# Performance work log

Measured on AMD Instinct MI355X. Metric: run time of the kernel, lower is better.

## Reference

```python
import jax, jax.numpy as jnp
import numpy as np

B, S, IN_F, OUT_F = 4, 2048, 4096, 4096
LUT_SIZE = 256


def setup_inputs() -> dict:
    key = jax.random.key(0)
    k_x, k_idx = jax.random.split(key, 2)
    x = jax.random.normal(k_x, (B, S, IN_F), dtype=jnp.float32)
    # quantized weight codes, one per weight element (uint8 in torch; int32 here)
    grid_indices = jax.random.randint(k_idx, (OUT_F, IN_F), 0, LUT_SIZE, dtype=jnp.int32)
    # per-output-row scale, initialized to ones as in the module
    scale = jnp.ones((OUT_F, 1), dtype=jnp.float32)
    # PRIMAL_LUT: 256-entry linear manifold codebook
    lut = jnp.linspace(-1.0, 1.0, LUT_SIZE, dtype=jnp.float32)
    return {"x": x, "grid_indices": grid_indices, "scale": scale, "lut": lut}


def reference(x, grid_indices, scale, lut):
    # dequant: gather codebook entries per weight element, scale per output row
    weights = lut[grid_indices] * scale            # [OUT_F, IN_F]
    # F.linear(x, weights) == x @ weights.T
    return jnp.einsum('bsi,oi->bso', x, weights)   # [B, S, OUT_F]
```

## Files before the change

kernel.cpp:

```cpp
#include <hip/hip_runtime.h>
#include <hip/hip_bf16.h>


#define M_DIM 8192
#define N_DIM 4096
#define K_DIM 4096
#define BM 128
#define BN 128
#define BK 64

typedef __bf16 bf16x8 __attribute__((ext_vector_type(8)));
typedef float floatx4 __attribute__((ext_vector_type(4)));
typedef int intx4 __attribute__((ext_vector_type(4)));
typedef unsigned short ushortx8 __attribute__((ext_vector_type(8)));

__device__ __forceinline__ unsigned short f2bf(float f) {
    return __builtin_bit_cast(unsigned short, (__bf16)f);
}

__device__ __forceinline__ void async_load16(const void* g, void* l) {
    auto gp = reinterpret_cast<const __attribute__((address_space(1))) void*>(
        reinterpret_cast<unsigned long long>(g));
    auto lp = reinterpret_cast<__attribute__((address_space(3))) void*>(
        static_cast<unsigned int>(reinterpret_cast<unsigned long long>(l)));
    __builtin_amdgcn_global_load_lds(gp, lp, 16, 0, 0);
}

__global__ __launch_bounds__(256) void prep(const float* __restrict__ x,
                                            unsigned short* __restrict__ xb,
                                            const int* __restrict__ idx,
                                            const float* __restrict__ scale,
                                            const float* __restrict__ lut,
                                            unsigned short* __restrict__ wb) {
    __shared__ float slut[256];
    if (blockIdx.x < 16384) {
        size_t i = ((size_t)blockIdx.x * 256 + threadIdx.x) * 8;
        floatx4 a = __builtin_nontemporal_load((const floatx4*)(x + i));
        floatx4 b = __builtin_nontemporal_load((const floatx4*)(x + i + 4));
        ushortx8 v;
        v[0] = f2bf(a[0]); v[1] = f2bf(a[1]); v[2] = f2bf(a[2]); v[3] = f2bf(a[3]);
        v[4] = f2bf(b[0]); v[5] = f2bf(b[1]); v[6] = f2bf(b[2]); v[7] = f2bf(b[3]);
        *(ushortx8*)(xb + i) = v;
    } else {
        if (threadIdx.x < 256) slut[threadIdx.x] = lut[threadIdx.x];
        __syncthreads();
        size_t i = ((size_t)(blockIdx.x - 16384) * 256 + threadIdx.x) * 8;
        int row = (int)(i >> 12);
        float s = scale[row];
        intx4 i0 = __builtin_nontemporal_load((const intx4*)(idx + i));
        intx4 i1 = __builtin_nontemporal_load((const intx4*)(idx + i + 4));
        ushortx8 v;
        v[0] = f2bf(slut[i0[0]] * s); v[1] = f2bf(slut[i0[1]] * s);
        v[2] = f2bf(slut[i0[2]] * s); v[3] = f2bf(slut[i0[3]] * s);
        v[4] = f2bf(slut[i1[0]] * s); v[5] = f2bf(slut[i1[1]] * s);
        v[6] = f2bf(slut[i1[2]] * s); v[7] = f2bf(slut[i1[3]] * s);
        *(ushortx8*)(wb + i) = v;
    }
}

__global__ __launch_bounds__(256) void gemm_bf16(const unsigned short* __restrict__ A,
                                                 const unsigned short* __restrict__ Bw,
                                                 float* __restrict__ C) {
    __shared__ __align__(16) unsigned short As[BM * BK];
    __shared__ __align__(16) unsigned short Bs[BN * BK];

    const int id = blockIdx.x;
    const int st = id >> 5;
    const int li = id & 31;
    const int m_blk = (st & 7) * 8 + (li & 7);
    const int n_blk = (st >> 3) * 4 + (li >> 3);
    const int m0 = m_blk * BM;
    const int n0 = n_blk * BN;

    const int t    = threadIdx.x;
    const int wave = t >> 6;
    const int lane = t & 63;

    const int mw   = (wave >> 1) * 64;
    const int nw   = (wave & 1) * 64;
    const int quad = lane >> 4;
    const int lcol = lane & 15;

    floatx4 acc[4][4];
#pragma unroll
    for (int i = 0; i < 4; i++)
#pragma unroll
        for (int j = 0; j < 4; j++) acc[i][j] = (floatx4)0.0f;

    const int rr = t >> 3;
    const int cc = t & 7;
    const int sw = (((cc - rr) & 7) << 3);
    unsigned short* AsB[4];
    unsigned short* BsB[4];
#pragma unroll
    for (int i = 0; i < 4; i++) {
        AsB[i] = As + (i * 32 + (wave << 3)) * BK;
        BsB[i] = Bs + (i * 32 + (wave << 3)) * BK;
    }

    const unsigned short* aG = A + (size_t)m0 * K_DIM;
    const unsigned short* bG = Bw + (size_t)n0 * K_DIM;

    for (int k0 = 0; k0 < K_DIM; k0 += BK) {
#pragma unroll
        for (int i = 0; i < 4; i++) {
            async_load16(aG + (size_t)(i * 32 + rr) * K_DIM + k0 + sw, AsB[i]);
            async_load16(bG + (size_t)(i * 32 + rr) * K_DIM + k0 + sw, BsB[i]);
        }
        __syncthreads();

#pragma unroll
        for (int ks = 0; ks < 2; ks++) {
            bf16x8 a[4], b[4];
#pragma unroll
            for (int mt = 0; mt < 4; mt++) {
                int R = mw + mt * 16 + lcol;
                int ch = (quad + ks * 4 + R) & 7;
                a[mt] = *(const bf16x8*)(As + R * BK + ch * 8);
            }
#pragma unroll
            for (int nt = 0; nt < 4; nt++) {
                int R = nw + nt * 16 + lcol;
                int ch = (quad + ks * 4 + R) & 7;
                b[nt] = *(const bf16x8*)(Bs + R * BK + ch * 8);
            }
#pragma unroll
            for (int mt = 0; mt < 4; mt++)
#pragma unroll
                for (int nt = 0; nt < 4; nt++)
                    acc[mt][nt] = __builtin_amdgcn_mfma_f32_16x16x32_bf16(
                        a[mt], b[nt], acc[mt][nt], 0, 0, 0);
        }
        __syncthreads();
    }

#pragma unroll
    for (int mt = 0; mt < 4; mt++) {
#pragma unroll
        for (int r = 0; r < 4; r++) {
            int row = m0 + mw + mt * 16 + quad * 4 + r;
            float* cr = C + (size_t)row * N_DIM + n0 + nw + lcol;
#pragma unroll
            for (int nt = 0; nt < 4; nt++)
                __builtin_nontemporal_store(acc[mt][nt][r], cr + nt * 16);
        }
    }
}

__global__ __launch_bounds__(256) void gemm_fallback(const float* __restrict__ x,
                                                     const int* __restrict__ idx,
                                                     const float* __restrict__ scale,
                                                     const float* __restrict__ lut,
                                                     float* __restrict__ C) {
    __shared__ float xs[16][17];
    __shared__ float wsm[16][17];
    const int tx = threadIdx.x & 15;
    const int ty = threadIdx.x >> 4;
    const int m = blockIdx.y * 16 + ty;
    const int n = blockIdx.x * 16 + tx;
    float acc = 0.f;
    for (int k0 = 0; k0 < K_DIM; k0 += 16) {
        xs[ty][tx] = x[(size_t)m * K_DIM + k0 + tx];
        int wrow = blockIdx.x * 16 + ty;
        wsm[ty][tx] = lut[idx[(size_t)wrow * K_DIM + k0 + tx]] * scale[wrow];
        __syncthreads();
#pragma unroll
        for (int kk = 0; kk < 16; kk++) acc += xs[ty][kk] * wsm[tx][kk];
        __syncthreads();
    }
    C[(size_t)m * N_DIM + n] = acc;
}

extern "C" void kernel_launch(void* const* d_in, const int* in_sizes, int n_in,
                              void* d_out, int out_size, void* d_ws, size_t ws_size,
                              hipStream_t stream) {
    const float* x     = (const float*)d_in[0];
    const int*   gidx  = (const int*)d_in[1];
    const float* scale = (const float*)d_in[2];
    const float* lut   = (const float*)d_in[3];
    float*       out   = (float*)d_out;

    const size_t needA = (size_t)M_DIM * K_DIM * sizeof(unsigned short);
    const size_t needW = (size_t)N_DIM * K_DIM * sizeof(unsigned short);

    if (ws_size >= needA + needW) {
        unsigned short* Ab = (unsigned short*)d_ws;
        unsigned short* Wb = Ab + (size_t)M_DIM * K_DIM;
        prep<<<24576, 256, 0, stream>>>(x, Ab, gidx, scale, lut, Wb);
        gemm_bf16<<<(M_DIM / BM) * (N_DIM / BN), 256, 0, stream>>>(Ab, Wb, out);
    } else {
        dim3 grid(N_DIM / 16, M_DIM / 16);
        gemm_fallback<<<grid, 16 * 16, 0, stream>>>(x, gidx, scale, lut, out);
    }
}
```

Before: 528.1 us.

## Replace 128x128 GEMM with 256x256 eight-wave double-buffered pipelined kernel

Replaces the single-buffered 128x128 bf16 GEMM with a 256x256-tile kernel using 512 threads and 128KB of dynamic LDS. Shared memory is double-buffered and loaded in half-tile stages that are interleaved with MFMA blocks under explicit barriers, sched_barriers, vmcnt waits and setprio. Blocks are remapped across XCDs. The aim is to raise arithmetic intensity per tile and hide global-to-LDS latency behind matrix math. In exchange, register pressure and barrier count go up, and the grid drops to one large workgroup per CU.

```diff
diff --git a/kernel.cpp b/kernel.cpp
--- a/kernel.cpp
+++ b/kernel.cpp
@@ -5,9 +5,10 @@
 #define M_DIM 8192
 #define N_DIM 4096
 #define K_DIM 4096
-#define BM 128
-#define BN 128
+#define BM 256
+#define BN 256
 #define BK 64
+#define NKT (K_DIM / BK)
 
 typedef __bf16 bf16x8 __attribute__((ext_vector_type(8)));
 typedef float floatx4 __attribute__((ext_vector_type(4)));
@@ -58,88 +59,159 @@
     }
 }
 
-__global__ __launch_bounds__(256) void gemm_bf16(const unsigned short* __restrict__ A,
-                                                 const unsigned short* __restrict__ Bw,
-                                                 float* __restrict__ C) {
-    __shared__ __align__(16) unsigned short As[BM * BK];
-    __shared__ __align__(16) unsigned short Bs[BN * BK];
+
+#define SBAR() __builtin_amdgcn_sched_barrier(0)
+#define BARRIER()                          \
+    do {                                   \
+        asm volatile("" ::: "memory");     \
+        __builtin_amdgcn_s_barrier();      \
+        asm volatile("" ::: "memory");     \
+    } while (0)
+#define VMCNT4() asm volatile("s_waitcnt vmcnt(4)" ::: "memory")
+
+#define MMA(HM, HN, BR)                                                          \
+    do {                                                                         \
+        __builtin_amdgcn_s_setprio(1);                                           \
+        _Pragma("unroll") for (int mt = 0; mt < 4; mt++)                         \
+            _Pragma("unroll") for (int nt = 0; nt < 2; nt++)                     \
+                _Pragma("unroll") for (int ks = 0; ks < 2; ks++)                 \
+                    acc[(HM) * 4 + mt][(HN) * 2 + nt] =                          \
+                        __builtin_amdgcn_mfma_f32_16x16x32_bf16(                 \
+                            aReg[mt][ks], BR[nt][ks],                            \
+                            acc[(HM) * 4 + mt][(HN) * 2 + nt], 0, 0, 0);         \
+        __builtin_amdgcn_s_setprio(0);                                           \
+    } while (0)
+
+__global__ __launch_bounds__(512, 2) void gemm256(const unsigned short* __restrict__ A,
+                                                  const unsigned short* __restrict__ Bw,
+                                                  float* __restrict__ C) {
+    extern __shared__ unsigned short lds[];
+    unsigned short* __restrict__ As = lds;
+    unsigned short* __restrict__ Bs = lds + 2 * BM * BK;
 
     const int id = blockIdx.x;
-    const int st = id >> 5;
-    const int li = id & 31;
-    const int m_blk = (st & 7) * 8 + (li & 7);
-    const int n_blk = (st >> 3) * 4 + (li >> 3);
-    const int m0 = m_blk * BM;
-    const int n0 = n_blk * BN;
+    const int wg = (id & 7) * 64 + (id >> 3);
+    const int m0 = (wg >> 4) * BM;
+    const int n0 = (wg & 15) * BN;
 
     const int t    = threadIdx.x;
-    const int wave = t >> 6;
     const int lane = t & 63;
-
-    const int mw   = (wave >> 1) * 64;
-    const int nw   = (wave & 1) * 64;
+    const int w    = t >> 6;
+    const int wm   = w >> 2;
+    const int wn   = w & 3;
     const int quad = lane >> 4;
     const int lcol = lane & 15;
 
-    floatx4 acc[4][4];
-#pragma unroll
-    for (int i = 0; i < 4; i++)
+    const int sRow = t >> 3;
+    const int gOff = (((t & 7) - sRow) & 7) * 8;
+
+    floatx4 acc[8][4];
+#pragma unroll
+    for (int i = 0; i < 8; i++)
 #pragma unroll
         for (int j = 0; j < 4; j++) acc[i][j] = (floatx4)0.0f;
 
-    const int rr = t >> 3;
-    const int cc = t & 7;
-    const int sw = (((cc - rr) & 7) << 3);
-    unsigned short* AsB[4];
-    unsigned short* BsB[4];
-#pragma unroll
-    for (int i = 0; i < 4; i++) {
-        AsB[i] = As + (i * 32 + (wave << 3)) * BK;
-        BsB[i] = Bs + (i * 32 + (wave << 3)) * BK;
-    }
-
-    const unsigned short* aG = A + (size_t)m0 * K_DIM;
-    const unsigned short* bG = Bw + (size_t)n0 * K_DIM;
-
-    for (int k0 = 0; k0 < K_DIM; k0 += BK) {
-#pragma unroll
-        for (int i = 0; i < 4; i++) {
-            async_load16(aG + (size_t)(i * 32 + rr) * K_DIM + k0 + sw, AsB[i]);
-            async_load16(bG + (size_t)(i * 32 + rr) * K_DIM + k0 + sw, BsB[i]);
-        }
-        __syncthreads();
-
-#pragma unroll
-        for (int ks = 0; ks < 2; ks++) {
-            bf16x8 a[4], b[4];
-#pragma unroll
-            for (int mt = 0; mt < 4; mt++) {
-                int R = mw + mt * 16 + lcol;
-                int ch = (quad + ks * 4 + R) & 7;
-                a[mt] = *(const bf16x8*)(As + R * BK + ch * 8);
+    bf16x8 aReg[4][2], b0Reg[2][2], b1Reg[2][2];
+
+    auto stageA = [&](int buf, int half, int kt) {
+        const int ko = (kt & (NKT - 1)) * BK + gOff;
+#pragma unroll
+        for (int c = 0; c < 2; c++) {
+            int r = c * 128 + half * 64 + sRow;
+            const unsigned short* s = A + (size_t)(m0 + r) * K_DIM + ko;
+            unsigned short* d = As + buf * (BM * BK) + r * BK + (t & 7) * 8;
+            async_load16(s, d);
+        }
+    };
+    auto stageB = [&](int buf, int half, int kt) {
+        const int ko = (kt & (NKT - 1)) * BK + gOff;
+#pragma unroll
+        for (int c = 0; c < 2; c++) {
+            int r = c * 128 + ((sRow >> 5) * 64) + half * 32 + (sRow & 31);
+            const unsigned short* s = Bw + (size_t)(n0 + r) * K_DIM + ko;
+            unsigned short* d = Bs + buf * (BN * BK) + r * BK + (t & 7) * 8;
+            async_load16(s, d);
+        }
+    };
+
+    auto lda = [&](int buf, int hm) {
+#pragma unroll
+        for (int mt = 0; mt < 4; mt++) {
+            int R = wm * 128 + hm * 64 + mt * 16 + lcol;
+#pragma unroll
+            for (int ks = 0; ks < 2; ks++) {
+                int ch = (ks * 4 + quad + R) & 7;
+                aReg[mt][ks] = *(const bf16x8*)(As + buf * (BM * BK) + R * BK + ch * 8);
             }
-#pragma unroll
-            for (int nt = 0; nt < 4; nt++) {
-                int R = nw + nt * 16 + lcol;
-                int ch = (quad + ks * 4 + R) & 7;
-                b[nt] = *(const bf16x8*)(Bs + R * BK + ch * 8);
+        }
+    };
+    auto ldb = [&](bf16x8(&bR)[2][2], int buf, int hn) {
+#pragma unroll
+        for (int nt = 0; nt < 2; nt++) {
+            int R = wn * 64 + hn * 32 + nt * 16 + lcol;
+#pragma unroll
+            for (int ks = 0; ks < 2; ks++) {
+                int ch = (ks * 4 + quad + R) & 7;
+                bR[nt][ks] = *(const bf16x8*)(Bs + buf * (BN * BK) + R * BK + ch * 8);
             }
-#pragma unroll
-            for (int mt = 0; mt < 4; mt++)
-#pragma unroll
-                for (int nt = 0; nt < 4; nt++)
-                    acc[mt][nt] = __builtin_amdgcn_mfma_f32_16x16x32_bf16(
-                        a[mt], b[nt], acc[mt][nt], 0, 0, 0);
-        }
-        __syncthreads();
-    }
-
-#pragma unroll
-    for (int mt = 0; mt < 4; mt++) {
+        }
+    };
+
+    stageA(0, 0, 0); stageB(0, 0, 0);
+    stageA(0, 1, 0); stageB(0, 1, 0);
+    stageA(1, 0, 1); stageB(1, 0, 1);
+    VMCNT4();
+    BARRIER();
+    SBAR();
+
+    for (int i = 0; i < NKT / 2; i++) {
+        const int T0 = 2 * i;
+        lda(0, 0); ldb(b0Reg, 0, 0);
+        stageA(1, 1, T0 + 1);
+        SBAR(); BARRIER();
+        MMA(0, 0, b0Reg);
+        SBAR(); BARRIER(); SBAR();
+        ldb(b1Reg, 0, 1);
+        stageB(1, 1, T0 + 1);
+        SBAR(); BARRIER();
+        MMA(0, 1, b1Reg);
+        SBAR(); BARRIER(); SBAR();
+        lda(0, 1);
+        stageA(0, 0, T0 + 2);
+        SBAR(); BARRIER();
+        MMA(1, 0, b0Reg);
+        SBAR(); BARRIER(); SBAR();
+        stageB(0, 0, T0 + 2);
+        SBAR(); BARRIER();
+        MMA(1, 1, b1Reg);
+        SBAR(); VMCNT4(); BARRIER(); SBAR();
+        lda(1, 0); ldb(b0Reg, 1, 0);
+        stageA(0, 1, T0 + 2);
+        SBAR(); BARRIER();
+        MMA(0, 0, b0Reg);
+        SBAR(); BARRIER(); SBAR();
+        ldb(b1Reg, 1, 1);
+        stageB(0, 1, T0 + 2);
+        SBAR(); BARRIER();
+        MMA(0, 1, b1Reg);
+        SBAR(); BARRIER(); SBAR();
+        lda(1, 1);
+        stageA(1, 0, T0 + 3);
+        SBAR(); BARRIER();
+        MMA(1, 0, b0Reg);
+        SBAR(); BARRIER(); SBAR();
+        stageB(1, 0, T0 + 3);
+        SBAR(); BARRIER();
+        MMA(1, 1, b1Reg);
+        SBAR(); VMCNT4(); BARRIER(); SBAR();
+    }
+
+#pragma unroll
+    for (int mt = 0; mt < 8; mt++) {
 #pragma unroll
         for (int r = 0; r < 4; r++) {
-            int row = m0 + mw + mt * 16 + quad * 4 + r;
-            float* cr = C + (size_t)row * N_DIM + n0 + nw + lcol;
+            int row = m0 + wm * 128 + mt * 16 + quad * 4 + r;
+            float* cr = C + (size_t)row * N_DIM + n0 + wn * 64 + lcol;
 #pragma unroll
             for (int nt = 0; nt < 4; nt++)
                 __builtin_nontemporal_store(acc[mt][nt][r], cr + nt * 16);
@@ -184,10 +256,17 @@
     const size_t needW = (size_t)N_DIM * K_DIM * sizeof(unsigned short);
 
     if (ws_size >= needA + needW) {
+        static bool s_attr = false;
+        if (!s_attr) {
+            (void)hipFuncSetAttribute((const void*)gemm256,
+                                      hipFuncAttributeMaxDynamicSharedMemorySize,
+                                      131072);
+            s_attr = true;
+        }
         unsigned short* Ab = (unsigned short*)d_ws;
         unsigned short* Wb = Ab + (size_t)M_DIM * K_DIM;
         prep<<<24576, 256, 0, stream>>>(x, Ab, gidx, scale, lut, Wb);
-        gemm_bf16<<<(M_DIM / BM) * (N_DIM / BN), 256, 0, stream>>>(Ab, Wb, out);
+        gemm256<<<(M_DIM / BM) * (N_DIM / BN), 512, 131072, stream>>>(Ab, Wb, out);
     } else {
         dim3 grid(N_DIM / 16, M_DIM / 16);
         gemm_fallback<<<grid, 16 * 16, 0, stream>>>(x, gidx, scale, lut, out);
```

Result: faster. 472.8 us (-10.5%).
